# Optimization experiments

Hardware: AMD Instinct MI355X
Metric: run time of the kernel (lower is better)

Reference implementation:

```python
import jax, jax.numpy as jnp
import numpy as np

B, S, EMB, H = 2, 2048, 1024, 16
D = EMB // H  # per-head dim = 64
SCALE = 1.0 / np.sqrt(D).astype(np.float32)


def setup_inputs() -> dict:
    key = jax.random.key(0)
    ks = jax.random.split(key, 11)
    lim = 1.0 / np.sqrt(EMB).astype(np.float32)  # torch Linear default init range
    def lin(kw, kb):
        W = jax.random.uniform(kw, (EMB, EMB), jnp.float32, -lim, lim)
        b = jax.random.uniform(kb, (EMB,), jnp.float32, -lim, lim)
        return W, b
    Wq, bq = lin(ks[0], ks[1])
    Wk, bk = lin(ks[2], ks[3])
    Wv, bv = lin(ks[4], ks[5])
    Wo, bo = lin(ks[6], ks[7])
    xq = jax.random.normal(ks[8], (B, S, EMB), jnp.float32)
    xk = jax.random.normal(ks[9], (B, S, EMB), jnp.float32)
    xv = jax.random.normal(ks[10], (B, S, EMB), jnp.float32)
    mask = jnp.tril(jnp.ones((S, S), dtype=jnp.int32))  # causal mask; 0 -> blocked
    return {"xq": xq, "xk": xk, "xv": xv, "mask": mask,
            "Wq": Wq, "bq": bq, "Wk": Wk, "bk": bk,
            "Wv": Wv, "bv": bv, "Wo": Wo, "bo": bo}


def reference(xq, xk, xv, mask, Wq, bq, Wk, bk, Wv, bv, Wo, bo):
    # Projections (torch Linear: x @ W.T + b), then split heads: [B,S,E] -> [B,H,S,D]
    def split_heads(x):
        return x.reshape(B, S, H, D).transpose(0, 2, 1, 3)
    Q = split_heads(xq @ Wq.T + bq)
    K = split_heads(xk @ Wk.T + bk)
    V = split_heads(xv @ Wv.T + bv)
    scores = jnp.einsum("bhqd,bhkd->bhqk", Q, K) * SCALE  # [B,H,S,S]
    scores = jnp.where(mask[None, None, :, :] == 0, jnp.float32(-1e9), scores)
    attn = jax.nn.softmax(scores, axis=-1)  # softmax over key axis (dim=2 per-head in torch)
    res = jnp.einsum("bhqk,bhkd->bhqd", attn, V)
    res = res.transpose(0, 2, 1, 3).reshape(B, S, EMB)  # merge heads back (same slicing layout)
    return res @ Wo.T + bo
```

## Files before the change

### kernel.cpp

```cpp
#include <hip/hip_runtime.h>
#include <hip/hip_bf16.h>

#define BB   2
#define SS   2048
#define EMBD 1024
#define NH   16
#define HD   64
#define SCALE 0.125f
#define NEG_BIG (-1e30f)

typedef __bf16 bf16;
typedef float  floatx4 __attribute__((ext_vector_type(4)));
typedef __bf16 bf16x4  __attribute__((ext_vector_type(4)));
typedef __bf16 bf16x8  __attribute__((ext_vector_type(8)));

typedef const __attribute__((address_space(1))) void* gas_ptr;
typedef __attribute__((address_space(3))) void*       las_ptr;

__device__ __forceinline__ void gl_lds16(const void* g, void* l) {
    __builtin_amdgcn_global_load_lds((gas_ptr)g, (las_ptr)l, 16, 0, 0);
}

__device__ __forceinline__ bf16x8 cvt8(const float* p) {
    bf16x8 o;
#pragma unroll
    for (int j = 0; j < 8; j++) o[j] = (bf16)p[j];
    return o;
}

__global__ __launch_bounds__(256) void cvt_all(
    const float* __restrict__ xq, const float* __restrict__ xk,
    const float* __restrict__ xv, const float* __restrict__ Wq,
    const float* __restrict__ Wk, const float* __restrict__ Wv,
    const float* __restrict__ Wo, bf16* __restrict__ xqo,
    bf16* __restrict__ xko, bf16* __restrict__ xvo, bf16* __restrict__ Wqo,
    bf16* __restrict__ Wko, bf16* __restrict__ Wvo, bf16* __restrict__ Woo) {
    const int y = blockIdx.y;
    const float* src;
    bf16* dst;
    size_t n;
    const size_t NX = (size_t)BB * SS * EMBD;
    const size_t NW = (size_t)EMBD * EMBD;
    switch (y) {
        case 0: src = xq; dst = xqo; n = NX; break;
        case 1: src = xk; dst = xko; n = NX; break;
        case 2: src = xv; dst = xvo; n = NX; break;
        case 3: src = Wq; dst = Wqo; n = NW; break;
        case 4: src = Wk; dst = Wko; n = NW; break;
        case 5: src = Wv; dst = Wvo; n = NW; break;
        default: src = Wo; dst = Woo; n = NW; break;
    }
    const size_t stride = (size_t)gridDim.x * blockDim.x * 4;
    for (size_t i = ((size_t)blockIdx.x * blockDim.x + threadIdx.x) * 4;
         i < n; i += stride) {
        floatx4 v = *(const floatx4*)(src + i);
        bf16x4 o = {(bf16)v[0], (bf16)v[1], (bf16)v[2], (bf16)v[3]};
        *(bf16x4*)(dst + i) = o;
    }
}

template <int MODE>
__device__ __forceinline__ void gemm_body(const bf16* __restrict__ A,
                                          const bf16* __restrict__ W,
                                          const float* __restrict__ bias,
                                          void* __restrict__ Ov,
                                          int mBase, int nBase) {
    __shared__ __align__(16) char smem[32768];
    bf16* As = (bf16*)smem;
    bf16* Bs = (bf16*)(smem + 16384);

    const int t = threadIdx.x;
    const int l = t & 63, w = t >> 6;
    const int lm = l & 15, lq = l >> 4;
    const int K = 1024;
    const int wm = (w >> 1) * 64, wn = (w & 1) * 64;

    const floatx4 zero = {0.f, 0.f, 0.f, 0.f};
    floatx4 acc[4][4];
#pragma unroll
    for (int i = 0; i < 4; i++)
#pragma unroll
        for (int j = 0; j < 4; j++) acc[i][j] = zero;

    for (int kb = 0; kb < K; kb += 64) {
        __syncthreads();
#pragma unroll
        for (int i = 0; i < 4; i++) {
            int half = i >> 1;
            int rem  = (i & 1) * 256 + t;
            int row  = rem >> 2;
            int col  = half * 32 + (rem & 3) * 8;
            const bf16* ga = A + (size_t)(mBase + row) * K + kb + col;
            const bf16* gb = W + (size_t)(nBase + row) * K + kb + col;
            char* la = (char*)As + (i * 256 + w * 64) * 16;
            char* lb = (char*)Bs + (i * 256 + w * 64) * 16;
            gl_lds16(ga, la);
            gl_lds16(gb, lb);
        }
        __syncthreads();

#pragma unroll
        for (int half = 0; half < 2; half++) {
            const bf16* Ah = As + half * 128 * 32;
            const bf16* Bh = Bs + half * 128 * 32;
            bf16x8 af[4], bfv[4];
#pragma unroll
            for (int f = 0; f < 4; f++) {
                int rowA = wm + f * 16 + lm;
                af[f] = *(const bf16x8*)&Ah[rowA * 32 + lq * 8];
                int rowB = wn + f * 16 + lm;
                bfv[f] = *(const bf16x8*)&Bh[rowB * 32 + lq * 8];
            }
            if (MODE == 2) {
#pragma unroll
                for (int i = 0; i < 4; i++)
#pragma unroll
                    for (int j = 0; j < 4; j++)
                        acc[i][j] = __builtin_amdgcn_mfma_f32_16x16x32_bf16(
                            bfv[i], af[j], acc[i][j], 0, 0, 0);
            } else {
#pragma unroll
                for (int fm = 0; fm < 4; fm++)
#pragma unroll
                    for (int fn = 0; fn < 4; fn++)
                        acc[fm][fn] =
                            __builtin_amdgcn_mfma_f32_16x16x32_bf16(
                                af[fm], bfv[fn], acc[fm][fn], 0, 0, 0);
            }
        }
    }

    __syncthreads();
    float* rp = (float*)smem + w * (16 * 68);

    if (MODE != 2) {
        float bvv[4];
#pragma unroll
        for (int fn = 0; fn < 4; fn++)
            bvv[fn] = bias[nBase + wn + fn * 16 + lm];
#pragma unroll
        for (int fm = 0; fm < 4; fm++) {
#pragma unroll
            for (int fn = 0; fn < 4; fn++)
#pragma unroll
                for (int r = 0; r < 4; r++)
                    rp[(lq * 4 + r) * 68 + fn * 16 + lm] =
                        acc[fm][fn][r] + bvv[fn];
            if (MODE == 0) {
                int row2 = l >> 3, col8 = l & 7;
                int h = (nBase + wn) >> 6;
#pragma unroll
                for (int p = 0; p < 2; p++) {
                    int row = p * 8 + row2;
                    int m = mBase + wm + fm * 16 + row;
                    int b = m >> 11, s = m & 2047;
                    bf16x8 o = cvt8(&rp[row * 68 + col8 * 8]);
                    *(bf16x8*)((bf16*)Ov +
                               (((size_t)(b * NH + h)) * SS + s) * HD +
                               col8 * 8) = o;
                }
            } else {
                int c4 = l & 15;
#pragma unroll
                for (int p = 0; p < 4; p++) {
                    int row = p * 4 + (l >> 4);
                    int m = mBase + wm + fm * 16 + row;
                    floatx4 o = *(const floatx4*)&rp[row * 68 + c4 * 4];
                    *(floatx4*)((float*)Ov + (size_t)m * EMBD + nBase + wn +
                                c4 * 4) = o;
                }
            }
        }
    } else {
        const int b = (mBase + wm) >> 11;
        const int sbase = (mBase + wm) & 2047;
#pragma unroll
        for (int i = 0; i < 4; i++) {
            float bv[4];
#pragma unroll
            for (int r = 0; r < 4; r++)
                bv[r] = bias[nBase + wn + i * 16 + lq * 4 + r];
#pragma unroll
            for (int j = 0; j < 4; j++)
#pragma unroll
                for (int r = 0; r < 4; r++)
                    rp[(lq * 4 + r) * 68 + j * 16 + lm] =
                        acc[i][j][r] + bv[r];
            int row2 = l >> 3, col8 = l & 7;
#pragma unroll
            for (int p = 0; p < 2; p++) {
                int row = p * 8 + row2;
                int n = nBase + wn + i * 16 + row;
                int h = n >> 6, d = n & 63;
                bf16x8 o = cvt8(&rp[row * 68 + col8 * 8]);
                *(bf16x8*)((bf16*)Ov +
                           ((size_t)(b * NH + h) * HD + d) * SS + sbase +
                           col8 * 8) = o;
            }
        }
    }
}

__global__ __launch_bounds__(256, 2) void gemm_qkv(
    const bf16* __restrict__ xq, const bf16* __restrict__ xk,
    const bf16* __restrict__ xv, const bf16* __restrict__ Wq,
    const bf16* __restrict__ Wk, const bf16* __restrict__ Wv,
    const float* __restrict__ bq, const float* __restrict__ bk,
    const float* __restrict__ bv, bf16* __restrict__ Qo,
    bf16* __restrict__ Ko, bf16* __restrict__ Vo) {
    const int z = blockIdx.z;
    if (z == 0)
        gemm_body<0>(xq, Wq, bq, Qo, blockIdx.y * 128, blockIdx.x * 128);
    else if (z == 1)
        gemm_body<0>(xk, Wk, bk, Ko, blockIdx.y * 128, blockIdx.x * 128);
    else
        gemm_body<2>(xv, Wv, bv, Vo, blockIdx.y * 128, blockIdx.x * 128);
}

__global__ __launch_bounds__(256, 2) void gemm_out(
    const bf16* __restrict__ A, const bf16* __restrict__ W,
    const float* __restrict__ bias, float* __restrict__ O) {
    gemm_body<1>(A, W, bias, O, blockIdx.y * 128, blockIdx.x * 128);
}

__global__ __launch_bounds__(256, 2) void attn_fwd(
    const bf16* __restrict__ Qg, const bf16* __restrict__ Kg,
    const bf16* __restrict__ Vtg, bf16* __restrict__ Oatt) {
    __shared__ __align__(16) bf16 Ks[64 * 72];
    __shared__ __align__(16) bf16 VT[64 * 72];
    __shared__ __align__(16) bf16 Ps[4][16 * 72];

    const int t = threadIdx.x;
    const int l = t & 63, w = t >> 6;
    const int lm = l & 15, lq = l >> 4;
    const int x = blockIdx.x;
    const int kk = x >> 3;
    const int bh = ((kk & 3) << 3) | (x & 7);
    const int qx = kk >> 2;
    const size_t kbase = (size_t)bh * SS * HD;
    const size_t vbase = (size_t)bh * HD * SS;
    const int b = bh >> 4, h = bh & 15;
    const floatx4 zero = {0.f, 0.f, 0.f, 0.f};

#pragma unroll
    for (int job = 0; job < 2; ++job) {
        const int qt = job ? (31 - qx) : qx;

        bf16x8 qa0, qa1;
        {
            const bf16* qp =
                Qg + kbase + (size_t)(qt * 64 + w * 16 + lm) * HD + lq * 8;
            qa0 = *(const bf16x8*)qp;
            qa1 = *(const bf16x8*)(qp + 32);
        }

        float m_i = NEG_BIG, l_i = 0.f;
        floatx4 od[4];
#pragma unroll
        for (int dt = 0; dt < 4; dt++) od[dt] = zero;

        const int qglob = qt * 64 + w * 16 + lm;

        bf16x8 kreg[2], vreg[2];
#pragma unroll
        for (int i = 0; i < 2; i++) {
            int idx = i * 256 + t;
            int row = idx >> 3;
            int col = (idx & 7) * 8;
            kreg[i] = *(const bf16x8*)(Kg + kbase + (size_t)row * HD + col);
            vreg[i] = *(const bf16x8*)(Vtg + vbase + (size_t)row * SS + col);
        }

        for (int kt = 0; kt <= qt; ++kt) {
            __syncthreads();
#pragma unroll
            for (int i = 0; i < 2; i++) {
                int idx = i * 256 + t;
                int row = idx >> 3;
                int col = (idx & 7) * 8;
                *(bf16x8*)&Ks[row * 72 + col] = kreg[i];
                *(bf16x8*)&VT[row * 72 + col] = vreg[i];
            }
            __syncthreads();
            if (kt < qt) {
#pragma unroll
                for (int i = 0; i < 2; i++) {
                    int idx = i * 256 + t;
                    int row = idx >> 3;
                    int col = (idx & 7) * 8;
                    kreg[i] = *(const bf16x8*)(
                        Kg + kbase + (size_t)((kt + 1) * 64 + row) * HD + col);
                    vreg[i] = *(const bf16x8*)(
                        Vtg + vbase + (size_t)row * SS + (kt + 1) * 64 + col);
                }
            }

            floatx4 sc[4];
#pragma unroll
            for (int j0 = 0; j0 < 4; j0++) {
                int rowK = j0 * 16 + lm;
                bf16x8 k0 = *(const bf16x8*)&Ks[rowK * 72 + lq * 8];
                bf16x8 k1 = *(const bf16x8*)&Ks[rowK * 72 + 32 + lq * 8];
                floatx4 z = zero;
                z = __builtin_amdgcn_mfma_f32_16x16x32_bf16(k0, qa0, z, 0, 0,
                                                            0);
                z = __builtin_amdgcn_mfma_f32_16x16x32_bf16(k1, qa1, z, 0, 0,
                                                            0);
                sc[j0] = z;
            }
#pragma unroll
            for (int j0 = 0; j0 < 4; j0++)
#pragma unroll
                for (int r = 0; r < 4; r++) {
                    float v = sc[j0][r] * SCALE;
                    if (kt == qt) {
                        int key = kt * 64 + j0 * 16 + lq * 4 + r;
                        if (key > qglob) v = NEG_BIG;
                    }
                    sc[j0][r] = v;
                }
            float mt = sc[0][0];
#pragma unroll
            for (int j0 = 0; j0 < 4; j0++)
#pragma unroll
                for (int r = 0; r < 4; r++) mt = fmaxf(mt, sc[j0][r]);
            mt = fmaxf(mt, __shfl_xor(mt, 16));
            mt = fmaxf(mt, __shfl_xor(mt, 32));
            float mnew = fmaxf(m_i, mt);
            float alpha = __expf(m_i - mnew);
            m_i = mnew;
            float ps = 0.f;
#pragma unroll
            for (int j0 = 0; j0 < 4; j0++)
#pragma unroll
                for (int r = 0; r < 4; r++) {
                    float p = __expf(sc[j0][r] - mnew);
                    sc[j0][r] = p;
                    ps += p;
                }
            ps += __shfl_xor(ps, 16);
            ps += __shfl_xor(ps, 32);
            l_i = l_i * alpha + ps;
#pragma unroll
            for (int j0 = 0; j0 < 4; j0++) {
                bf16x4 pk = {(bf16)sc[j0][0], (bf16)sc[j0][1],
                             (bf16)sc[j0][2], (bf16)sc[j0][3]};
                *(bf16x4*)&Ps[w][lm * 72 + j0 * 16 + lq * 4] = pk;
            }
            float a0 = __shfl(alpha, lq * 4 + 0);
            float a1 = __shfl(alpha, lq * 4 + 1);
            float a2 = __shfl(alpha, lq * 4 + 2);
            float a3 = __shfl(alpha, lq * 4 + 3);
#pragma unroll
            for (int dt = 0; dt < 4; dt++) {
                od[dt][0] *= a0;
                od[dt][1] *= a1;
                od[dt][2] *= a2;
                od[dt][3] *= a3;
            }
            bf16x8 pa0 = *(const bf16x8*)&Ps[w][lm * 72 + lq * 8];
            bf16x8 pa1 = *(const bf16x8*)&Ps[w][lm * 72 + 32 + lq * 8];
#pragma unroll
            for (int dt = 0; dt < 4; dt++) {
                int rowD = dt * 16 + lm;
                bf16x8 v0 = *(const bf16x8*)&VT[rowD * 72 + lq * 8];
                bf16x8 v1 = *(const bf16x8*)&VT[rowD * 72 + 32 + lq * 8];
                od[dt] = __builtin_amdgcn_mfma_f32_16x16x32_bf16(pa0, v0,
                                                                 od[dt], 0, 0,
                                                                 0);
                od[dt] = __builtin_amdgcn_mfma_f32_16x16x32_bf16(pa1, v1,
                                                                 od[dt], 0, 0,
                                                                 0);
            }
        }

        float lr0 = __shfl(l_i, lq * 4 + 0);
        float lr1 = __shfl(l_i, lq * 4 + 1);
        float lr2 = __shfl(l_i, lq * 4 + 2);
        float lr3 = __shfl(l_i, lq * 4 + 3);
        float lr[4] = {lr0, lr1, lr2, lr3};
#pragma unroll
        for (int dt = 0; dt < 4; dt++) {
#pragma unroll
            for (int r = 0; r < 4; r++) {
                int s = qt * 64 + w * 16 + lq * 4 + r;
                float v = od[dt][r] / lr[r];
                Oatt[((size_t)(b * SS + s)) * EMBD + h * HD + dt * 16 + lm] =
                    (bf16)v;
            }
        }
    }
}

extern "C" void kernel_launch(void* const* d_in, const int* in_sizes, int n_in,
                              void* d_out, int out_size, void* d_ws,
                              size_t ws_size, hipStream_t stream) {
    const float* xq = (const float*)d_in[0];
    const float* xk = (const float*)d_in[1];
    const float* xv = (const float*)d_in[2];
    const float* Wq = (const float*)d_in[4];
    const float* bq = (const float*)d_in[5];
    const float* Wk = (const float*)d_in[6];
    const float* bk = (const float*)d_in[7];
    const float* Wv = (const float*)d_in[8];
    const float* bv = (const float*)d_in[9];
    const float* Wo = (const float*)d_in[10];
    const float* bo = (const float*)d_in[11];
    float* out = (float*)d_out;

    const size_t NX = (size_t)BB * SS * EMBD;
    const size_t NW = (size_t)EMBD * EMBD;
    bf16* Qw  = (bf16*)d_ws;
    bf16* Kw  = Qw + NX;
    bf16* Vw  = Kw + NX;
    bf16* Aw  = Vw + NX;
    bf16* xqb = Aw + NX;
    bf16* xkb = xqb + NX;
    bf16* xvb = xkb + NX;
    bf16* Wqb = xvb + NX;
    bf16* Wkb = Wqb + NW;
    bf16* Wvb = Wkb + NW;
    bf16* Wob = Wvb + NW;

    cvt_all<<<dim3(1024, 7), 256, 0, stream>>>(xq, xk, xv, Wq, Wk, Wv, Wo,
                                               xqb, xkb, xvb, Wqb, Wkb, Wvb,
                                               Wob);
    gemm_qkv<<<dim3(8, 32, 3), 256, 0, stream>>>(xqb, xkb, xvb, Wqb, Wkb, Wvb,
                                                 bq, bk, bv, Qw, Kw, Vw);
    attn_fwd<<<dim3(512), 256, 0, stream>>>(Qw, Kw, Vw, Aw);
    gemm_out<<<dim3(8, 32), 256, 0, stream>>>(Aw, Wob, bo, out);
}
```

Before: 240.6 us.

## Fold softmax scale into Q, split attention jobs, smaller out-proj tiles

Folds the softmax scale and log2(e) into the Q projection epilogue so attention uses exp2f without a per-score multiply. Attention now launches one block per query tile instead of pairing two tiles per block, scheduling the longest causal tiles first, and raises launch_bounds occupancy to 4 blocks per SM. The output GEMM is templated to a 64-row M tile, doubling its grid. Together these aim for better load balance and occupancy; the 64-row tile costs some reuse of the weight tile.

```diff
diff --git a/kernel.cpp b/kernel.cpp
--- a/kernel.cpp
+++ b/kernel.cpp
@@ -6,7 +6,7 @@
 #define EMBD 1024
 #define NH   16
 #define HD   64
-#define SCALE 0.125f
+#define QSCALE 0.18033688011112042f
 #define NEG_BIG (-1e30f)
 
 typedef __bf16 bf16;
@@ -59,68 +59,76 @@
     }
 }
 
-template <int MODE>
+template <int MODE, int FM>
 __device__ __forceinline__ void gemm_body(const bf16* __restrict__ A,
                                           const bf16* __restrict__ W,
                                           const float* __restrict__ bias,
                                           void* __restrict__ Ov,
-                                          int mBase, int nBase) {
-    __shared__ __align__(16) char smem[32768];
+                                          int mBase, int nBase, float oscale) {
+    constexpr int BM = 32 * FM;
+    constexpr int ABYTES = BM * 64 * 2;
+    constexpr int STG = ABYTES + 128 * 64 * 2;
+    constexpr int SMEMSZ = (STG > 17408) ? STG : 17408;
+    __shared__ __align__(16) char smem[SMEMSZ];
     bf16* As = (bf16*)smem;
-    bf16* Bs = (bf16*)(smem + 16384);
+    bf16* Bs = (bf16*)(smem + ABYTES);
 
     const int t = threadIdx.x;
     const int l = t & 63, w = t >> 6;
     const int lm = l & 15, lq = l >> 4;
     const int K = 1024;
-    const int wm = (w >> 1) * 64, wn = (w & 1) * 64;
+    const int wm = (w >> 1) * (16 * FM), wn = (w & 1) * 64;
 
     const floatx4 zero = {0.f, 0.f, 0.f, 0.f};
-    floatx4 acc[4][4];
-#pragma unroll
-    for (int i = 0; i < 4; i++)
+    floatx4 acc[FM][4];
+#pragma unroll
+    for (int i = 0; i < FM; i++)
 #pragma unroll
         for (int j = 0; j < 4; j++) acc[i][j] = zero;
 
     for (int kb = 0; kb < K; kb += 64) {
         __syncthreads();
+#pragma unroll
+        for (int ia = 0; ia < FM; ia++) {
+            int half = ia / (FM / 2 > 0 ? FM / 2 : 1);
+            int rem  = (ia % (FM / 2 > 0 ? FM / 2 : 1)) * 256 + t;
+            int row  = rem >> 2;
+            int col  = half * 32 + (rem & 3) * 8;
+            gl_lds16(A + (size_t)(mBase + row) * K + kb + col,
+                     (char*)As + (ia * 256 + w * 64) * 16);
+        }
 #pragma unroll
         for (int i = 0; i < 4; i++) {
             int half = i >> 1;
             int rem  = (i & 1) * 256 + t;
             int row  = rem >> 2;
             int col  = half * 32 + (rem & 3) * 8;
-            const bf16* ga = A + (size_t)(mBase + row) * K + kb + col;
-            const bf16* gb = W + (size_t)(nBase + row) * K + kb + col;
-            char* la = (char*)As + (i * 256 + w * 64) * 16;
-            char* lb = (char*)Bs + (i * 256 + w * 64) * 16;
-            gl_lds16(ga, la);
-            gl_lds16(gb, lb);
+            gl_lds16(W + (size_t)(nBase + row) * K + kb + col,
+                     (char*)Bs + (i * 256 + w * 64) * 16);
         }
         __syncthreads();
 
 #pragma unroll
         for (int half = 0; half < 2; half++) {
-            const bf16* Ah = As + half * 128 * 32;
+            const bf16* Ah = As + half * BM * 32;
             const bf16* Bh = Bs + half * 128 * 32;
-            bf16x8 af[4], bfv[4];
-#pragma unroll
-            for (int f = 0; f < 4; f++) {
-                int rowA = wm + f * 16 + lm;
-                af[f] = *(const bf16x8*)&Ah[rowA * 32 + lq * 8];
-                int rowB = wn + f * 16 + lm;
-                bfv[f] = *(const bf16x8*)&Bh[rowB * 32 + lq * 8];
-            }
+            bf16x8 af[FM], bfv[4];
+#pragma unroll
+            for (int f = 0; f < FM; f++)
+                af[f] = *(const bf16x8*)&Ah[(wm + f * 16 + lm) * 32 + lq * 8];
+#pragma unroll
+            for (int f = 0; f < 4; f++)
+                bfv[f] = *(const bf16x8*)&Bh[(wn + f * 16 + lm) * 32 + lq * 8];
             if (MODE == 2) {
 #pragma unroll
                 for (int i = 0; i < 4; i++)
 #pragma unroll
-                    for (int j = 0; j < 4; j++)
-                        acc[i][j] = __builtin_amdgcn_mfma_f32_16x16x32_bf16(
-                            bfv[i], af[j], acc[i][j], 0, 0, 0);
+                    for (int j = 0; j < FM; j++)
+                        acc[j][i] = __builtin_amdgcn_mfma_f32_16x16x32_bf16(
+                            bfv[i], af[j], acc[j][i], 0, 0, 0);
             } else {
 #pragma unroll
-                for (int fm = 0; fm < 4; fm++)
+                for (int fm = 0; fm < FM; fm++)
 #pragma unroll
                     for (int fn = 0; fn < 4; fn++)
                         acc[fm][fn] =
@@ -139,13 +147,13 @@
         for (int fn = 0; fn < 4; fn++)
             bvv[fn] = bias[nBase + wn + fn * 16 + lm];
 #pragma unroll
-        for (int fm = 0; fm < 4; fm++) {
+        for (int fm = 0; fm < FM; fm++) {
 #pragma unroll
             for (int fn = 0; fn < 4; fn++)
 #pragma unroll
                 for (int r = 0; r < 4; r++)
                     rp[(lq * 4 + r) * 68 + fn * 16 + lm] =
-                        acc[fm][fn][r] + bvv[fn];
+                        (acc[fm][fn][r] + bvv[fn]) * oscale;
             if (MODE == 0) {
                 int row2 = l >> 3, col8 = l & 7;
                 int h = (nBase + wn) >> 6;
@@ -181,11 +189,11 @@
             for (int r = 0; r < 4; r++)
                 bv[r] = bias[nBase + wn + i * 16 + lq * 4 + r];
 #pragma unroll
-            for (int j = 0; j < 4; j++)
+            for (int j = 0; j < FM; j++)
 #pragma unroll
                 for (int r = 0; r < 4; r++)
                     rp[(lq * 4 + r) * 68 + j * 16 + lm] =
-                        acc[i][j][r] + bv[r];
+                        acc[j][i][r] + bv[r];
             int row2 = l >> 3, col8 = l & 7;
 #pragma unroll
             for (int p = 0; p < 2; p++) {
@@ -210,20 +218,23 @@
     bf16* __restrict__ Ko, bf16* __restrict__ Vo) {
     const int z = blockIdx.z;
     if (z == 0)
-        gemm_body<0>(xq, Wq, bq, Qo, blockIdx.y * 128, blockIdx.x * 128);
+        gemm_body<0, 4>(xq, Wq, bq, Qo, blockIdx.y * 128, blockIdx.x * 128,
+                        QSCALE);
     else if (z == 1)
-        gemm_body<0>(xk, Wk, bk, Ko, blockIdx.y * 128, blockIdx.x * 128);
+        gemm_body<0, 4>(xk, Wk, bk, Ko, blockIdx.y * 128, blockIdx.x * 128,
+                        1.0f);
     else
-        gemm_body<2>(xv, Wv, bv, Vo, blockIdx.y * 128, blockIdx.x * 128);
+        gemm_body<2, 4>(xv, Wv, bv, Vo, blockIdx.y * 128, blockIdx.x * 128,
+                        1.0f);
 }
 
 __global__ __launch_bounds__(256, 2) void gemm_out(
     const bf16* __restrict__ A, const bf16* __restrict__ W,
     const float* __restrict__ bias, float* __restrict__ O) {
-    gemm_body<1>(A, W, bias, O, blockIdx.y * 128, blockIdx.x * 128);
-}
-
-__global__ __launch_bounds__(256, 2) void attn_fwd(
+    gemm_body<1, 2>(A, W, bias, O, blockIdx.y * 64, blockIdx.x * 128, 1.0f);
+}
+
+__global__ __launch_bounds__(256, 4) void attn_fwd(
     const bf16* __restrict__ Qg, const bf16* __restrict__ Kg,
     const bf16* __restrict__ Vtg, bf16* __restrict__ Oatt) {
     __shared__ __align__(16) bf16 Ks[64 * 72];
@@ -234,160 +245,148 @@
     const int l = t & 63, w = t >> 6;
     const int lm = l & 15, lq = l >> 4;
     const int x = blockIdx.x;
-    const int kk = x >> 3;
-    const int bh = ((kk & 3) << 3) | (x & 7);
-    const int qx = kk >> 2;
+    const int qt = 31 - (x >> 5);
+    const int bh = (((x >> 3) & 3) << 3) | (x & 7);
     const size_t kbase = (size_t)bh * SS * HD;
     const size_t vbase = (size_t)bh * HD * SS;
     const int b = bh >> 4, h = bh & 15;
     const floatx4 zero = {0.f, 0.f, 0.f, 0.f};
 
-#pragma unroll
-    for (int job = 0; job < 2; ++job) {
-        const int qt = job ? (31 - qx) : qx;
-
-        bf16x8 qa0, qa1;
-        {
-            const bf16* qp =
-                Qg + kbase + (size_t)(qt * 64 + w * 16 + lm) * HD + lq * 8;
-            qa0 = *(const bf16x8*)qp;
-            qa1 = *(const bf16x8*)(qp + 32);
-        }
-
-        float m_i = NEG_BIG, l_i = 0.f;
-        floatx4 od[4];
-#pragma unroll
-        for (int dt = 0; dt < 4; dt++) od[dt] = zero;
-
-        const int qglob = qt * 64 + w * 16 + lm;
-
-        bf16x8 kreg[2], vreg[2];
+    bf16x8 qa0, qa1;
+    {
+        const bf16* qp =
+            Qg + kbase + (size_t)(qt * 64 + w * 16 + lm) * HD + lq * 8;
+        qa0 = *(const bf16x8*)qp;
+        qa1 = *(const bf16x8*)(qp + 32);
+    }
+
+    float m_i = NEG_BIG, l_i = 0.f;
+    floatx4 od[4];
+#pragma unroll
+    for (int dt = 0; dt < 4; dt++) od[dt] = zero;
+
+    const int qglob = qt * 64 + w * 16 + lm;
+
+    bf16x8 kreg[2], vreg[2];
+#pragma unroll
+    for (int i = 0; i < 2; i++) {
+        int idx = i * 256 + t;
+        int row = idx >> 3;
+        int col = (idx & 7) * 8;
+        kreg[i] = *(const bf16x8*)(Kg + kbase + (size_t)row * HD + col);
+        vreg[i] = *(const bf16x8*)(Vtg + vbase + (size_t)row * SS + col);
+    }
+
+    for (int kt = 0; kt <= qt; ++kt) {
+        __syncthreads();
 #pragma unroll
         for (int i = 0; i < 2; i++) {
             int idx = i * 256 + t;
             int row = idx >> 3;
             int col = (idx & 7) * 8;
-            kreg[i] = *(const bf16x8*)(Kg + kbase + (size_t)row * HD + col);
-            vreg[i] = *(const bf16x8*)(Vtg + vbase + (size_t)row * SS + col);
-        }
-
-        for (int kt = 0; kt <= qt; ++kt) {
-            __syncthreads();
+            *(bf16x8*)&Ks[row * 72 + col] = kreg[i];
+            *(bf16x8*)&VT[row * 72 + col] = vreg[i];
+        }
+        __syncthreads();
+        if (kt < qt) {
 #pragma unroll
             for (int i = 0; i < 2; i++) {
                 int idx = i * 256 + t;
                 int row = idx >> 3;
                 int col = (idx & 7) * 8;
-                *(bf16x8*)&Ks[row * 72 + col] = kreg[i];
-                *(bf16x8*)&VT[row * 72 + col] = vreg[i];
+                kreg[i] = *(const bf16x8*)(
+                    Kg + kbase + (size_t)((kt + 1) * 64 + row) * HD + col);
+                vreg[i] = *(const bf16x8*)(
+                    Vtg + vbase + (size_t)row * SS + (kt + 1) * 64 + col);
             }
-            __syncthreads();
-            if (kt < qt) {
-#pragma unroll
-                for (int i = 0; i < 2; i++) {
-                    int idx = i * 256 + t;
-                    int row = idx >> 3;
-                    int col = (idx & 7) * 8;
-                    kreg[i] = *(const bf16x8*)(
-                        Kg + kbase + (size_t)((kt + 1) * 64 + row) * HD + col);
-                    vreg[i] = *(const bf16x8*)(
-                        Vtg + vbase + (size_t)row * SS + (kt + 1) * 64 + col);
+        }
+
+        floatx4 sc[4];
+#pragma unroll
+        for (int j0 = 0; j0 < 4; j0++) {
+            int rowK = j0 * 16 + lm;
+            bf16x8 k0 = *(const bf16x8*)&Ks[rowK * 72 + lq * 8];
+            bf16x8 k1 = *(const bf16x8*)&Ks[rowK * 72 + 32 + lq * 8];
+            floatx4 z = zero;
+            z = __builtin_amdgcn_mfma_f32_16x16x32_bf16(k0, qa0, z, 0, 0, 0);
+            z = __builtin_amdgcn_mfma_f32_16x16x32_bf16(k1, qa1, z, 0, 0, 0);
+            sc[j0] = z;
+        }
+        if (kt == qt) {
+#pragma unroll
+            for (int j0 = 0; j0 < 4; j0++)
+#pragma unroll
+                for (int r = 0; r < 4; r++) {
+                    int key = kt * 64 + j0 * 16 + lq * 4 + r;
+                    if (key > qglob) sc[j0][r] = NEG_BIG;
                 }
+        }
+        float mt = sc[0][0];
+#pragma unroll
+        for (int j0 = 0; j0 < 4; j0++)
+#pragma unroll
+            for (int r = 0; r < 4; r++) mt = fmaxf(mt, sc[j0][r]);
+        mt = fmaxf(mt, __shfl_xor(mt, 16));
+        mt = fmaxf(mt, __shfl_xor(mt, 32));
+        float mnew = fmaxf(m_i, mt);
+        float alpha = exp2f(m_i - mnew);
+        m_i = mnew;
+        float ps = 0.f;
+#pragma unroll
+        for (int j0 = 0; j0 < 4; j0++)
+#pragma unroll
+            for (int r = 0; r < 4; r++) {
+                float p = exp2f(sc[j0][r] - mnew);
+                sc[j0][r] = p;
+                ps += p;
             }
-
-            floatx4 sc[4];
-#pragma unroll
-            for (int j0 = 0; j0 < 4; j0++) {
-                int rowK = j0 * 16 + lm;
-                bf16x8 k0 = *(const bf16x8*)&Ks[rowK * 72 + lq * 8];
-                bf16x8 k1 = *(const bf16x8*)&Ks[rowK * 72 + 32 + lq * 8];
-                floatx4 z = zero;
-                z = __builtin_amdgcn_mfma_f32_16x16x32_bf16(k0, qa0, z, 0, 0,
-                                                            0);
-                z = __builtin_amdgcn_mfma_f32_16x16x32_bf16(k1, qa1, z, 0, 0,
-                                                            0);
-                sc[j0] = z;
-            }
-#pragma unroll
-            for (int j0 = 0; j0 < 4; j0++)
-#pragma unroll
-                for (int r = 0; r < 4; r++) {
-                    float v = sc[j0][r] * SCALE;
-                    if (kt == qt) {
-                        int key = kt * 64 + j0 * 16 + lq * 4 + r;
-                        if (key > qglob) v = NEG_BIG;
-                    }
-                    sc[j0][r] = v;
-                }
-            float mt = sc[0][0];
-#pragma unroll
-            for (int j0 = 0; j0 < 4; j0++)
-#pragma unroll
-                for (int r = 0; r < 4; r++) mt = fmaxf(mt, sc[j0][r]);
-            mt = fmaxf(mt, __shfl_xor(mt, 16));
-            mt = fmaxf(mt, __shfl_xor(mt, 32));
-            float mnew = fmaxf(m_i, mt);
-            float alpha = __expf(m_i - mnew);
-            m_i = mnew;
-            float ps = 0.f;
-#pragma unroll
-            for (int j0 = 0; j0 < 4; j0++)
-#pragma unroll
-                for (int r = 0; r < 4; r++) {
-                    float p = __expf(sc[j0][r] - mnew);
-                    sc[j0][r] = p;
-                    ps += p;
-                }
-            ps += __shfl_xor(ps, 16);
-            ps += __shfl_xor(ps, 32);
-            l_i = l_i * alpha + ps;
-#pragma unroll
-            for (int j0 = 0; j0 < 4; j0++) {
-                bf16x4 pk = {(bf16)sc[j0][0], (bf16)sc[j0][1],
-                             (bf16)sc[j0][2], (bf16)sc[j0][3]};
-                *(bf16x4*)&Ps[w][lm * 72 + j0 * 16 + lq * 4] = pk;
-            }
-            float a0 = __shfl(alpha, lq * 4 + 0);
-            float a1 = __shfl(alpha, lq * 4 + 1);
-            float a2 = __shfl(alpha, lq * 4 + 2);
-            float a3 = __shfl(alpha, lq * 4 + 3);
-#pragma unroll
-            for (int dt = 0; dt < 4; dt++) {
-                od[dt][0] *= a0;
-                od[dt][1] *= a1;
-                od[dt][2] *= a2;
-                od[dt][3] *= a3;
-            }
-            bf16x8 pa0 = *(const bf16x8*)&Ps[w][lm * 72 + lq * 8];
-            bf16x8 pa1 = *(const bf16x8*)&Ps[w][lm * 72 + 32 + lq * 8];
-#pragma unroll
-            for (int dt = 0; dt < 4; dt++) {
-                int rowD = dt * 16 + lm;
-                bf16x8 v0 = *(const bf16x8*)&VT[rowD * 72 + lq * 8];
-                bf16x8 v1 = *(const bf16x8*)&VT[rowD * 72 + 32 + lq * 8];
-                od[dt] = __builtin_amdgcn_mfma_f32_16x16x32_bf16(pa0, v0,
-                                                                 od[dt], 0, 0,
-                                                                 0);
-                od[dt] = __builtin_amdgcn_mfma_f32_16x16x32_bf16(pa1, v1,
-                                                                 od[dt], 0, 0,
-                                                                 0);
-            }
-        }
-
-        float lr0 = __shfl(l_i, lq * 4 + 0);
-        float lr1 = __shfl(l_i, lq * 4 + 1);
-        float lr2 = __shfl(l_i, lq * 4 + 2);
-        float lr3 = __shfl(l_i, lq * 4 + 3);
-        float lr[4] = {lr0, lr1, lr2, lr3};
+        ps += __shfl_xor(ps, 16);
+        ps += __shfl_xor(ps, 32);
+        l_i = l_i * alpha + ps;
+#pragma unroll
+        for (int j0 = 0; j0 < 4; j0++) {
+            bf16x4 pk = {(bf16)sc[j0][0], (bf16)sc[j0][1], (bf16)sc[j0][2],
+                         (bf16)sc[j0][3]};
+            *(bf16x4*)&Ps[w][lm * 72 + j0 * 16 + lq * 4] = pk;
+        }
+        float a0 = __shfl(alpha, lq * 4 + 0);
+        float a1 = __shfl(alpha, lq * 4 + 1);
+        float a2 = __shfl(alpha, lq * 4 + 2);
+        float a3 = __shfl(alpha, lq * 4 + 3);
 #pragma unroll
         for (int dt = 0; dt < 4; dt++) {
-#pragma unroll
-            for (int r = 0; r < 4; r++) {
-                int s = qt * 64 + w * 16 + lq * 4 + r;
-                float v = od[dt][r] / lr[r];
-                Oatt[((size_t)(b * SS + s)) * EMBD + h * HD + dt * 16 + lm] =
-                    (bf16)v;
-            }
+            od[dt][0] *= a0;
+            od[dt][1] *= a1;
+            od[dt][2] *= a2;
+            od[dt][3] *= a3;
+        }
+        bf16x8 pa0 = *(const bf16x8*)&Ps[w][lm * 72 + lq * 8];
+        bf16x8 pa1 = *(const bf16x8*)&Ps[w][lm * 72 + 32 + lq * 8];
+#pragma unroll
+        for (int dt = 0; dt < 4; dt++) {
+            int rowD = dt * 16 + lm;
+            bf16x8 v0 = *(const bf16x8*)&VT[rowD * 72 + lq * 8];
+            bf16x8 v1 = *(const bf16x8*)&VT[rowD * 72 + 32 + lq * 8];
+            od[dt] = __builtin_amdgcn_mfma_f32_16x16x32_bf16(pa0, v0, od[dt],
+                                                             0, 0, 0);
+            od[dt] = __builtin_amdgcn_mfma_f32_16x16x32_bf16(pa1, v1, od[dt],
+                                                             0, 0, 0);
+        }
+    }
+
+    float lr0 = __shfl(l_i, lq * 4 + 0);
+    float lr1 = __shfl(l_i, lq * 4 + 1);
+    float lr2 = __shfl(l_i, lq * 4 + 2);
+    float lr3 = __shfl(l_i, lq * 4 + 3);
+    float lr[4] = {lr0, lr1, lr2, lr3};
+#pragma unroll
+    for (int dt = 0; dt < 4; dt++) {
+#pragma unroll
+        for (int r = 0; r < 4; r++) {
+            int s = qt * 64 + w * 16 + lq * 4 + r;
+            float v = od[dt][r] / lr[r];
+            Oatt[((size_t)(b * SS + s)) * EMBD + h * HD + dt * 16 + lm] =
+                (bf16)v;
         }
     }
 }
@@ -427,6 +426,6 @@
                                                Wob);
     gemm_qkv<<<dim3(8, 32, 3), 256, 0, stream>>>(xqb, xkb, xvb, Wqb, Wkb, Wvb,
                                                  bq, bk, bv, Qw, Kw, Vw);
-    attn_fwd<<<dim3(512), 256, 0, stream>>>(Qw, Kw, Vw, Aw);
-    gemm_out<<<dim3(8, 32), 256, 0, stream>>>(Aw, Wob, bo, out);
-}
+    attn_fwd<<<dim3(1024), 256, 0, stream>>>(Qw, Kw, Vw, Aw);
+    gemm_out<<<dim3(8, 64), 256, 0, stream>>>(Aw, Wob, bo, out);
+}
```

New measurement: 240.0 us. Within noise of the previous version (-0.2%).
